# Optimization experiments

Hardware: AMD Instinct MI355X
Metric: run time of the kernel (lower is better)

The kernel has to match this reference:

```python
import jax, jax.numpy as jnp
import numpy as np

NEMBEDS = 512
EMBED_DIM = 64


def setup_inputs() -> dict:
    key = jax.random.key(0)
    k1, k2 = jax.random.split(key)
    z_e = jax.random.normal(k1, (32, EMBED_DIM, 64, 64), dtype=jnp.float32)
    codebook = jax.random.uniform(
        k2, (NEMBEDS, EMBED_DIM), dtype=jnp.float32,
        minval=-1.0 / NEMBEDS, maxval=1.0 / NEMBEDS)
    return {"z_e": z_e, "codebook": codebook}


def reference(z_e, codebook):
    # NCHW -> NHWC, flatten spatial+batch into tokens
    z = jnp.transpose(z_e, (0, 2, 3, 1))          # [B,H,W,D]
    B, H, W, D = z.shape
    flat = z.reshape(-1, D)                        # [N,D]
    # squared L2 distances (argmin of ||.||_2 == argmin of ||.||_2^2)
    # expanded form avoids the [N,K,D] broadcast intermediate
    d2 = (jnp.sum(flat * flat, axis=-1, keepdims=True)
          - 2.0 * flat @ codebook.T
          + jnp.sum(codebook * codebook, axis=-1))  # [N,K]
    inds = jnp.argmin(d2, axis=1)                   # [N]
    # direct gather == one-hot matmul lookup
    z_q = codebook[inds].reshape(B, H, W, D)        # [B,H,W,D]
    # commitment + codebook loss, per-batch mean over H,W,D
    sg = jax.lax.stop_gradient
    vq_loss = (jnp.mean((sg(z) - z_q) ** 2, axis=(1, 2, 3))
               + 0.25 * jnp.mean((z - sg(z_q)) ** 2, axis=(1, 2, 3)))  # [B]
    # straight-through estimator
    z_q_st = z + sg(z_q - z)
    out = jnp.transpose(z_q_st, (0, 3, 1, 2))       # back to NCHW
    return out, vq_loss, inds[:, None]
```

## Files before the change

kernel.cpp:

```cpp
#include <hip/hip_runtime.h>

#define NEMB 512
#define DIM 64
#define NB 32
#define HW 4096
#define NTOK (NB * HW)
#define TPB 512
#define TOKBLK 512
#define BLOCKS (NTOK / TOKBLK)

typedef float f32x16 __attribute__((ext_vector_type(16)));
typedef short bf16x8 __attribute__((ext_vector_type(8)));

#define WS_PART 0
#define WS_SUMC 512
#define WS_CMAX 1024
#define WS_SCMAX 1025
#define WS_CH 1040
#define WS_CL (1040 + 16384)

__device__ __forceinline__ unsigned short f2bf(float f) {
    unsigned u = __float_as_uint(f);
    unsigned r = u + 0x7FFFu + ((u >> 16) & 1u);
    return (unsigned short)(r >> 16);
}
__device__ __forceinline__ float bf2f(unsigned short h) {
    return __uint_as_float((unsigned)h << 16);
}

__global__ void vq_prep(const float* __restrict__ cb, float* __restrict__ ws)
{
    __shared__ float redm[256], redsc[256];
    const int tid = threadIdx.x;
    float cmax_t = 0.f, scmax_t = 0.f;
    for (int rep = 0; rep < 2; ++rep) {
        int k = rep * 256 + tid;
        {
#pragma clang fp contract(off)
            float s = 0.f;
#pragma unroll
            for (int d = 0; d < DIM; ++d) {
                float v = cb[k * DIM + d];
                float p = v * v;
                s = s + p;
            }
            ws[WS_SUMC + k] = s;
            scmax_t = fmaxf(scmax_t, s);
        }
        unsigned* chp = (unsigned*)(ws + WS_CH) + k * 32;
        unsigned* clp = (unsigned*)(ws + WS_CL) + k * 32;
#pragma unroll
        for (int q = 0; q < 32; ++q) {
            float v0 = cb[k * DIM + 2 * q], v1 = cb[k * DIM + 2 * q + 1];
            cmax_t = fmaxf(cmax_t, fmaxf(fabsf(v0), fabsf(v1)));
            unsigned short h0 = f2bf(v0), h1 = f2bf(v1);
            unsigned short l0 = f2bf(v0 - bf2f(h0)), l1 = f2bf(v1 - bf2f(h1));
            chp[q] = (unsigned)h0 | ((unsigned)h1 << 16);
            clp[q] = (unsigned)l0 | ((unsigned)l1 << 16);
        }
    }
    redm[tid] = cmax_t; redsc[tid] = scmax_t;
    __syncthreads();
    for (int s = 128; s > 0; s >>= 1) {
        if (tid < s) {
            redm[tid]  = fmaxf(redm[tid],  redm[tid + s]);
            redsc[tid] = fmaxf(redsc[tid], redsc[tid + s]);
        }
        __syncthreads();
    }
    if (tid == 0) { ws[WS_CMAX] = redm[0]; ws[WS_SCMAX] = redsc[0]; }
}

__global__ __launch_bounds__(TPB, 2)
void vq_main(const float* __restrict__ z_e, const float* __restrict__ cb,
             const float* __restrict__ ws, float* __restrict__ out,
             float* __restrict__ loss_part, float* __restrict__ inds_out)
{
    __shared__ uint4 ch_s[NEMB * 9];
    __shared__ uint4 cl_s[NEMB * 9];
    __shared__ float sumc_s[NEMB];
    __shared__ float red_s[TPB];
    __shared__ float sc2[2];

    const int tid  = threadIdx.x;
    const int gid  = blockIdx.x;
    const int b    = gid >> 3;
    const int base = (gid & 7) * TOKBLK;
    const int w    = tid >> 6;
    const int l    = tid & 63;
    const int col  = l & 31;
    const int half = l >> 5;

    {
        const uint4* chg = (const uint4*)(ws + WS_CH);
        const uint4* clg = (const uint4*)(ws + WS_CL);
#pragma unroll
        for (int i = 0; i < 8; ++i) {
            int idx = i * TPB + tid;
            int c = idx >> 3, bd = idx & 7;
            int slot = (bd + c) & 7;
            ch_s[c * 9 + slot] = chg[idx];
            cl_s[c * 9 + slot] = clg[idx];
        }
        sumc_s[tid] = ws[WS_SUMC + tid];
        if (tid < 2) sc2[tid] = ws[WS_CMAX + tid];
    }

    const float* zb = z_e + (size_t)b * DIM * HW;
    const int t0 = base + w * 64;
    uint4 bzh[2][4], bzl[2][4];
    float l1p[2] = {0.f, 0.f}, szp[2] = {0.f, 0.f};
#pragma unroll
    for (int tt = 0; tt < 2; ++tt) {
        int tok = t0 + tt * 32 + col;
#pragma unroll
        for (int ks = 0; ks < 4; ++ks) {
            unsigned hh[8], ll[8];
#pragma unroll
            for (int j = 0; j < 8; ++j) {
                int d = 16 * ks + 8 * half + j;
                float v = zb[(size_t)d * HW + tok];
                l1p[tt] += fabsf(v);
                szp[tt] = fmaf(v, v, szp[tt]);
                unsigned short h = f2bf(v);
                unsigned short lo = f2bf(v - bf2f(h));
                hh[j] = h; ll[j] = lo;
            }
            bzh[tt][ks] = make_uint4(hh[0] | (hh[1] << 16), hh[2] | (hh[3] << 16),
                                     hh[4] | (hh[5] << 16), hh[6] | (hh[7] << 16));
            bzl[tt][ks] = make_uint4(ll[0] | (ll[1] << 16), ll[2] | (ll[3] << 16),
                                     ll[4] | (ll[5] << 16), ll[6] | (ll[7] << 16));
        }
    }
    float L1[2], SZ[2];
#pragma unroll
    for (int tt = 0; tt < 2; ++tt) {
        L1[tt] = l1p[tt] + __shfl_xor(l1p[tt], 32);
        SZ[tt] = szp[tt] + __shfl_xor(szp[tt], 32);
    }
    __syncthreads();

    const float cmax = sc2[0], scmax = sc2[1];
    float gapd[2];
#pragma unroll
    for (int tt = 0; tt < 2; ++tt)
        gapd[tt] = 1.2e-4f * cmax * L1[tt] + 0.5f * scmax + 1.2e-7f * SZ[tt] + 1e-6f;

    unsigned mask0[8], mask1[8];
#pragma unroll
    for (int i = 0; i < 8; ++i) { mask0[i] = 0u; mask1[i] = 0u; }
    float runm[2] = {-3.402823466e38f, -3.402823466e38f};

    for (int ct = 0; ct < 16; ++ct) {
        bf16x8 ah[4], al[4];
        const int c = 32 * ct + col;
        const int rowb = c * 9;
#pragma unroll
        for (int ks = 0; ks < 4; ++ks) {
            int slot = ((2 * ks + half) + c) & 7;
            uint4 u1 = ch_s[rowb + slot];
            uint4 u2 = cl_s[rowb + slot];
            ah[ks] = *(bf16x8*)&u1;
            al[ks] = *(bf16x8*)&u2;
        }
#pragma unroll
        for (int tt = 0; tt < 2; ++tt) {
            f32x16 acc = {0.f, 0.f, 0.f, 0.f, 0.f, 0.f, 0.f, 0.f,
                          0.f, 0.f, 0.f, 0.f, 0.f, 0.f, 0.f, 0.f};
#pragma unroll
            for (int ks = 0; ks < 4; ++ks)
                acc = __builtin_amdgcn_mfma_f32_32x32x16_bf16(ah[ks], *(bf16x8*)&bzh[tt][ks], acc, 0, 0, 0);
#pragma unroll
            for (int ks = 0; ks < 4; ++ks)
                acc = __builtin_amdgcn_mfma_f32_32x32x16_bf16(al[ks], *(bf16x8*)&bzh[tt][ks], acc, 0, 0, 0);
#pragma unroll
            for (int ks = 0; ks < 4; ++ks)
                acc = __builtin_amdgcn_mfma_f32_32x32x16_bf16(ah[ks], *(bf16x8*)&bzl[tt][ks], acc, 0, 0, 0);
            float m = acc[0];
#pragma unroll
            for (int r = 1; r < 16; ++r) m = fmaxf(m, acc[r]);
            float rm = fmaxf(tt == 0 ? runm[0] : runm[1], m);
            if (tt == 0) runm[0] = rm; else runm[1] = rm;
            float thr = rm - (tt == 0 ? gapd[0] : gapd[1]);
            unsigned bits = 0;
#pragma unroll
            for (int r = 0; r < 16; ++r)
                bits |= (acc[r] >= thr) ? (1u << r) : 0u;
            unsigned sh = bits << ((ct & 1) * 16);
            if (tt == 0) mask0[ct >> 1] |= sh; else mask1[ct >> 1] |= sh;
        }
    }

    unsigned om[8], xm[8];
#pragma unroll
    for (int i = 0; i < 8; ++i) {
        om[i] = half ? mask1[i] : mask0[i];
        xm[i] = __shfl_xor(half ? mask0[i] : mask1[i], 32);
    }

    const int hwme = base + tid;
    float z[DIM];
    float sumz;
    {
#pragma clang fp contract(off)
        sumz = 0.f;
#pragma unroll
        for (int d = 0; d < DIM; ++d) {
            float v = zb[(size_t)d * HW + hwme];
            z[d] = v;
            float p = v * v;
            sumz = sumz + p;
        }
    }

    float best = 3.402823466e38f;
    int bk = 0;
    for (int ct = 0; ct < 16; ++ct) {
        unsigned A = (om[ct >> 1] >> ((ct & 1) * 16)) & 0xFFFFu;
        unsigned B = (xm[ct >> 1] >> ((ct & 1) * 16)) & 0xFFFFu;
        unsigned wo = ((A & 0xFu)) | (((A >> 4) & 0xFu) << 8) |
                      (((A >> 8) & 0xFu) << 16) | (((A >> 12) & 0xFu) << 24);
        unsigned wx = ((B & 0xFu)) | (((B >> 4) & 0xFu) << 8) |
                      (((B >> 8) & 0xFu) << 16) | (((B >> 12) & 0xFu) << 24);
        unsigned wc = half ? ((wo << 4) | wx) : (wo | (wx << 4));
        while (wc) {
            int kk = __builtin_ctz(wc);
            wc &= wc - 1;
            int k = 32 * ct + kk;
            const float4* c4 = (const float4*)(cb + (size_t)k * DIM);
            float a0 = 0.f;
#pragma unroll
            for (int g = 0; g < DIM / 4; ++g) {
                float4 u = c4[g];
                a0 = fmaf(z[4 * g + 0], u.x, a0);
                a0 = fmaf(z[4 * g + 1], u.y, a0);
                a0 = fmaf(z[4 * g + 2], u.z, a0);
                a0 = fmaf(z[4 * g + 3], u.w, a0);
            }
            float d2 = (sumz - 2.0f * a0) + sumc_s[k];
            if (d2 < best) { best = d2; bk = k; }
        }
    }

    inds_out[(size_t)gid * TOKBLK + tid] = (float)bk;
    float* ob = out + (size_t)b * DIM * HW;
    float lsum = 0.f;
    const float4* q4 = (const float4*)(cb + (size_t)bk * DIM);
    {
#pragma clang fp contract(off)
#pragma unroll
        for (int g = 0; g < DIM / 4; ++g) {
            float4 qq = q4[g];
            float qv[4] = {qq.x, qq.y, qq.z, qq.w};
#pragma unroll
            for (int j = 0; j < 4; ++j) {
                int d = g * 4 + j;
                float t1 = qv[j] - z[d];
                ob[(size_t)d * HW + hwme] = z[d] + t1;
                float p = t1 * t1;
                lsum = lsum + p;
            }
        }
    }

    __syncthreads();
    red_s[tid] = lsum;
    __syncthreads();
#pragma unroll
    for (int s = 128; s > 0; s >>= 1) {
        if ((tid & 255) < s) red_s[tid] = red_s[tid] + red_s[tid + s];
        __syncthreads();
    }
    if (tid == 0)   loss_part[2 * gid]     = red_s[0];
    if (tid == 256) loss_part[2 * gid + 1] = red_s[256];
}

__global__ void vq_loss_final(const float* __restrict__ part,
                              float* __restrict__ loss_out)
{
    int b = threadIdx.x;
    if (b < NB) {
        float s = 0.f;
        for (int i = 0; i < 16; ++i)
            s = s + part[b * 16 + i];
        float m = s * (1.0f / (HW * DIM));
        loss_out[b] = m + 0.25f * m;
    }
}

extern "C" void kernel_launch(void* const* d_in, const int* in_sizes, int n_in,
                              void* d_out, int out_size, void* d_ws, size_t ws_size,
                              hipStream_t stream)
{
    const float* z_e = (const float*)d_in[0];
    const float* cb  = (const float*)d_in[1];

    float* out  = (float*)d_out;
    float* loss = out + (size_t)NB * DIM * HW;
    float* inds = loss + NB;
    float* ws   = (float*)d_ws;

    vq_prep<<<1, 256, 0, stream>>>(cb, ws);
    vq_main<<<BLOCKS, TPB, 0, stream>>>(z_e, cb, ws, out, ws + WS_PART, inds);
    vq_loss_final<<<1, 64, 0, stream>>>(ws + WS_PART, loss);
}
```

Measured before the change: 97.44 us.

## Drop codebook low-bf16 term, split codebook in-kernel, raise occupancy bound

Removes the codebook low-part bf16 split and its MFMA pass, so only hi(c)·hi(z) and hi(c)·lo(z) are computed. The candidate gap is widened to absorb the larger error, and exact candidates are resolved later. Codebook bf16 conversion and the max-abs/max-sumsq reductions move from the single-block prep kernel into each main block, and LDS use is halved. Launch bounds go from 2 to 4 blocks per CU. The risk is more candidates surviving to exact rescoring, plus redundant per-block codebook conversion.

Result: slower. 100.6 us (+3.3%).

```diff
diff --git a/kernel.cpp b/kernel.cpp
--- a/kernel.cpp
+++ b/kernel.cpp
@@ -12,13 +12,6 @@
 typedef float f32x16 __attribute__((ext_vector_type(16)));
 typedef short bf16x8 __attribute__((ext_vector_type(8)));
 
-#define WS_PART 0
-#define WS_SUMC 512
-#define WS_CMAX 1024
-#define WS_SCMAX 1025
-#define WS_CH 1040
-#define WS_CL (1040 + 16384)
-
 __device__ __forceinline__ unsigned short f2bf(float f) {
     unsigned u = __float_as_uint(f);
     unsigned r = u + 0x7FFFu + ((u >> 16) & 1u);
@@ -28,59 +21,30 @@
     return __uint_as_float((unsigned)h << 16);
 }
 
-__global__ void vq_prep(const float* __restrict__ cb, float* __restrict__ ws)
-{
-    __shared__ float redm[256], redsc[256];
-    const int tid = threadIdx.x;
-    float cmax_t = 0.f, scmax_t = 0.f;
-    for (int rep = 0; rep < 2; ++rep) {
-        int k = rep * 256 + tid;
-        {
+__global__ void vq_prep(const float* __restrict__ cb, float* __restrict__ sumc)
+{
+    int k = blockIdx.x * 256 + threadIdx.x;
+    if (k < NEMB) {
 #pragma clang fp contract(off)
-            float s = 0.f;
-#pragma unroll
-            for (int d = 0; d < DIM; ++d) {
-                float v = cb[k * DIM + d];
-                float p = v * v;
-                s = s + p;
-            }
-            ws[WS_SUMC + k] = s;
-            scmax_t = fmaxf(scmax_t, s);
-        }
-        unsigned* chp = (unsigned*)(ws + WS_CH) + k * 32;
-        unsigned* clp = (unsigned*)(ws + WS_CL) + k * 32;
-#pragma unroll
-        for (int q = 0; q < 32; ++q) {
-            float v0 = cb[k * DIM + 2 * q], v1 = cb[k * DIM + 2 * q + 1];
-            cmax_t = fmaxf(cmax_t, fmaxf(fabsf(v0), fabsf(v1)));
-            unsigned short h0 = f2bf(v0), h1 = f2bf(v1);
-            unsigned short l0 = f2bf(v0 - bf2f(h0)), l1 = f2bf(v1 - bf2f(h1));
-            chp[q] = (unsigned)h0 | ((unsigned)h1 << 16);
-            clp[q] = (unsigned)l0 | ((unsigned)l1 << 16);
-        }
-    }
-    redm[tid] = cmax_t; redsc[tid] = scmax_t;
-    __syncthreads();
-    for (int s = 128; s > 0; s >>= 1) {
-        if (tid < s) {
-            redm[tid]  = fmaxf(redm[tid],  redm[tid + s]);
-            redsc[tid] = fmaxf(redsc[tid], redsc[tid + s]);
-        }
-        __syncthreads();
-    }
-    if (tid == 0) { ws[WS_CMAX] = redm[0]; ws[WS_SCMAX] = redsc[0]; }
-}
-
-__global__ __launch_bounds__(TPB, 2)
+        float s = 0.f;
+#pragma unroll
+        for (int d = 0; d < DIM; ++d) {
+            float v = cb[k * DIM + d];
+            float p = v * v;
+            s = s + p;
+        }
+        sumc[k] = s;
+    }
+}
+
+__global__ __launch_bounds__(TPB, 4)
 void vq_main(const float* __restrict__ z_e, const float* __restrict__ cb,
-             const float* __restrict__ ws, float* __restrict__ out,
+             const float* __restrict__ sumc, float* __restrict__ out,
              float* __restrict__ loss_part, float* __restrict__ inds_out)
 {
     __shared__ uint4 ch_s[NEMB * 9];
-    __shared__ uint4 cl_s[NEMB * 9];
     __shared__ float sumc_s[NEMB];
     __shared__ float red_s[TPB];
-    __shared__ float sc2[2];
 
     const int tid  = threadIdx.x;
     const int gid  = blockIdx.x;
@@ -91,20 +55,28 @@
     const int col  = l & 31;
     const int half = l >> 5;
 
-    {
-        const uint4* chg = (const uint4*)(ws + WS_CH);
-        const uint4* clg = (const uint4*)(ws + WS_CL);
+    float cmax_l = 0.f;
+    {
+        const float4* cbg = (const float4*)cb;
 #pragma unroll
         for (int i = 0; i < 8; ++i) {
             int idx = i * TPB + tid;
             int c = idx >> 3, bd = idx & 7;
+            float4 v0 = cbg[idx * 2];
+            float4 v1 = cbg[idx * 2 + 1];
+            float vv[8] = {v0.x, v0.y, v0.z, v0.w, v1.x, v1.y, v1.z, v1.w};
+            unsigned wd[4];
+#pragma unroll
+            for (int q = 0; q < 4; ++q) {
+                cmax_l = fmaxf(cmax_l, fmaxf(fabsf(vv[2 * q]), fabsf(vv[2 * q + 1])));
+                wd[q] = (unsigned)f2bf(vv[2 * q]) | ((unsigned)f2bf(vv[2 * q + 1]) << 16);
+            }
             int slot = (bd + c) & 7;
-            ch_s[c * 9 + slot] = chg[idx];
-            cl_s[c * 9 + slot] = clg[idx];
-        }
-        sumc_s[tid] = ws[WS_SUMC + tid];
-        if (tid < 2) sc2[tid] = ws[WS_CMAX + tid];
-    }
+            ch_s[c * 9 + slot] = make_uint4(wd[0], wd[1], wd[2], wd[3]);
+        }
+    }
+    const float sc_v = sumc[tid];
+    sumc_s[tid] = sc_v;
 
     const float* zb = z_e + (size_t)b * DIM * HW;
     const int t0 = base + w * 64;
@@ -138,13 +110,28 @@
         L1[tt] = l1p[tt] + __shfl_xor(l1p[tt], 32);
         SZ[tt] = szp[tt] + __shfl_xor(szp[tt], 32);
     }
+
+    {
+        float cm = cmax_l, sm = sc_v;
+#pragma unroll
+        for (int off = 32; off; off >>= 1) {
+            cm = fmaxf(cm, __shfl_xor(cm, off));
+            sm = fmaxf(sm, __shfl_xor(sm, off));
+        }
+        if (l == 0) { red_s[w] = cm; red_s[8 + w] = sm; }
+    }
     __syncthreads();
-
-    const float cmax = sc2[0], scmax = sc2[1];
+    float cmax = red_s[0], scmax = red_s[8];
+#pragma unroll
+    for (int i = 1; i < 8; ++i) {
+        cmax  = fmaxf(cmax,  red_s[i]);
+        scmax = fmaxf(scmax, red_s[8 + i]);
+    }
+
     float gapd[2];
 #pragma unroll
     for (int tt = 0; tt < 2; ++tt)
-        gapd[tt] = 1.2e-4f * cmax * L1[tt] + 0.5f * scmax + 1.2e-7f * SZ[tt] + 1e-6f;
+        gapd[tt] = 8.0e-3f * cmax * L1[tt] + 0.5f * scmax + 1.2e-7f * SZ[tt] + 1e-6f;
 
     unsigned mask0[8], mask1[8];
 #pragma unroll
@@ -152,16 +139,14 @@
     float runm[2] = {-3.402823466e38f, -3.402823466e38f};
 
     for (int ct = 0; ct < 16; ++ct) {
-        bf16x8 ah[4], al[4];
+        bf16x8 ah[4];
         const int c = 32 * ct + col;
         const int rowb = c * 9;
 #pragma unroll
         for (int ks = 0; ks < 4; ++ks) {
             int slot = ((2 * ks + half) + c) & 7;
             uint4 u1 = ch_s[rowb + slot];
-            uint4 u2 = cl_s[rowb + slot];
             ah[ks] = *(bf16x8*)&u1;
-            al[ks] = *(bf16x8*)&u2;
         }
 #pragma unroll
         for (int tt = 0; tt < 2; ++tt) {
@@ -170,9 +155,6 @@
 #pragma unroll
             for (int ks = 0; ks < 4; ++ks)
                 acc = __builtin_amdgcn_mfma_f32_32x32x16_bf16(ah[ks], *(bf16x8*)&bzh[tt][ks], acc, 0, 0, 0);
-#pragma unroll
-            for (int ks = 0; ks < 4; ++ks)
-                acc = __builtin_amdgcn_mfma_f32_32x32x16_bf16(al[ks], *(bf16x8*)&bzh[tt][ks], acc, 0, 0, 0);
 #pragma unroll
             for (int ks = 0; ks < 4; ++ks)
                 acc = __builtin_amdgcn_mfma_f32_32x32x16_bf16(ah[ks], *(bf16x8*)&bzl[tt][ks], acc, 0, 0, 0);
@@ -298,9 +280,11 @@
     float* out  = (float*)d_out;
     float* loss = out + (size_t)NB * DIM * HW;
     float* inds = loss + NB;
-    float* ws   = (float*)d_ws;
-
-    vq_prep<<<1, 256, 0, stream>>>(cb, ws);
-    vq_main<<<BLOCKS, TPB, 0, stream>>>(z_e, cb, ws, out, ws + WS_PART, inds);
-    vq_loss_final<<<1, 64, 0, stream>>>(ws + WS_PART, loss);
-}
+
+    float* part  = (float*)d_ws;
+    float* sumcg = part + 512;
+
+    vq_prep<<<2, 256, 0, stream>>>(cb, sumcg);
+    vq_main<<<BLOCKS, TPB, 0, stream>>>(z_e, cb, sumcg, out, part, inds);
+    vq_loss_final<<<1, 64, 0, stream>>>(part, loss);
+}
```
